# Kernel tuning notes

Hardware: AMD Instinct MI355X
Metric: run time of the kernel (lower is better)

## Reference

```python
import jax, jax.numpy as jnp
import numpy as np

B, N0, D0, N1, D1 = 128, 64, 32, 64, 32
K = 65  # depthwise conv kernel size
SCALE = 5.0
FOCUS = 3.0
EPS_Z = float(jnp.finfo(jnp.float32).eps)


def setup_inputs() -> dict:
    key = jax.random.key(0)
    k1, k2, k3, kw, kc, kb = jax.random.split(key, 6)
    x1 = jax.random.normal(k1, (B, N0, D0), dtype=jnp.float32)
    x2 = jax.random.normal(k2, (B, N0, D0), dtype=jnp.float32)
    x3 = jax.random.normal(k3, (B, N0, D0), dtype=jnp.float32)
    # kaiming_normal_ on W [N1, N0, D0, D1]: fan_in = N0*D0*D1 per torch default on 4D
    fan_in = N0 * D0 * D1
    W = jax.random.normal(kw, (N1, N0, D0, D1), dtype=jnp.float32) * np.sqrt(2.0 / fan_in)
    # Conv1d(N1*D1, N1*D1, K, groups=N1): weight [out_ch, in_ch/groups, K]
    cin_g = D1
    bound = 1.0 / np.sqrt(cin_g * K)
    conv_w = jax.random.uniform(kc, (N1 * D1, cin_g, K), dtype=jnp.float32, minval=-bound, maxval=bound)
    conv_b = jax.random.uniform(kb, (N1 * D1,), dtype=jnp.float32, minval=-bound, maxval=bound)
    return {"x1": x1, "x2": x2, "x3": x3, "W": W, "conv_w": conv_w, "conv_b": conv_b}


def _transform(x, W):
    # x: [B, N0, D0], W: [N1, N0, D0, D1] -> u: [B, N1*D1, N0]
    u = jnp.einsum('bji,kjiz->bkjz', x, W)        # [B, N1, N0, D1]
    u = jnp.transpose(u, (0, 1, 3, 2))             # [B, N1, D1, N0]
    return u.reshape(u.shape[0], N1 * D1, N0)


def _focus(u):
    # ReLU kernel + focusing-factor renormalization along last dim
    u = jax.nn.relu(u) + 1e-6
    u = u / SCALE
    n = jnp.linalg.norm(u, axis=-1, keepdims=True)
    up = u ** FOCUS
    return up / jnp.linalg.norm(up, axis=-1, keepdims=True) * n


def _squash(x, eps=1e-20):
    norm = jnp.linalg.norm(x, axis=-1, keepdims=True)
    coef = 1.0 - 1.0 / (jnp.exp(norm) + eps)
    return coef * (x / (norm + eps))


def reference(x1, x2, x3, W, conv_w, conv_b):
    u1 = _focus(_transform(x1, W))  # [B, N1*D1, N0]
    u2 = _focus(_transform(x2, W))
    u3 = _focus(_transform(x3, W))
    z = 1.0 / (jnp.einsum('bic,bc->bi', u1, u1.sum(axis=1)) + EPS_Z)  # [B, N1*D1]
    kv = jnp.einsum('bjc,bjd->bcd', u2, u3)                           # [B, N0, N0]
    x = jnp.einsum('bic,bcd,bi->bid', u1, kv, z)                      # [B, N1*D1, N0]
    # grouped (depthwise-per-capsule) conv1d, 'same' padding
    y = jax.lax.conv_general_dilated(
        x, conv_w, window_strides=(1,), padding=[(K // 2, K // 2)],
        dimension_numbers=('NCH', 'OIH', 'NCH'), feature_group_count=N1)
    y = y + conv_b[None, :, None]
    out = (x + y).sum(axis=-1).reshape(-1, N1, D1)  # [B, N1, D1]
    return _squash(out)
```

## Files before the change

### kernel.cpp

```cpp
#include <hip/hip_runtime.h>
#include <cstddef>

#define NB 128
#define NT 64
#define ND 32
#define NG 64
#define NC 2048
#define KW 65
#define EPSZ 1.1920928955078125e-07f

#define OFF_URAW 0ull
#define SZ_URAW  (3ull * NB * NT * NC)
#define OFF_F    (OFF_URAW + SZ_URAW)
#define SZ_F     (3ull * NB * NC)
#define OFF_S1   (OFF_F + SZ_F)
#define SZ_S1    ((unsigned long long)NB * NT)
#define OFF_KV   (OFF_S1 + SZ_S1)
#define SZ_KV    ((unsigned long long)NB * NT * NT)

__device__ __forceinline__ float foc(float v, float fv) {
  float u = (fmaxf(v, 0.f) + 1e-6f) * 0.2f;
  return u * u * u * fv;
}

__global__ __launch_bounds__(256) void k_transform(
    const float* __restrict__ x1, const float* __restrict__ x2,
    const float* __restrict__ x3, const float* __restrict__ W,
    float* __restrict__ uraw) {
  int bid = blockIdx.x;
  int j   = bid & 63;
  int nt  = (bid >> 6) & 15;
  int inp = bid >> 10;
  const float* x = (inp == 0) ? x1 : ((inp == 1) ? x2 : x3);
  float* uout = uraw + (size_t)inp * ((size_t)NB * NT * NC);

  __shared__ float as[32][132];
  __shared__ float bs[32][132];
  int tid = threadIdx.x;

  {
    int b = tid >> 1, h = tid & 1;
    const float* xp = x + ((size_t)b * NT + j) * ND + h * 16;
#pragma unroll
    for (int q = 0; q < 4; ++q) {
      float4 v = *reinterpret_cast<const float4*>(xp + q * 4);
      int i0 = h * 16 + q * 4;
      as[i0 + 0][b] = v.x; as[i0 + 1][b] = v.y;
      as[i0 + 2][b] = v.z; as[i0 + 3][b] = v.w;
    }
  }
  {
    int kk = tid >> 6, u = tid & 63;
    int i = u >> 1, h = u & 1;
    const float* wp = W + (((size_t)(nt * 4 + kk) * NT + j) * ND + i) * ND + h * 16;
#pragma unroll
    for (int q = 0; q < 4; ++q) {
      float4 v = *reinterpret_cast<const float4*>(wp + q * 4);
      int c0 = kk * 32 + h * 16 + q * 4;
      bs[i][c0 + 0] = v.x; bs[i][c0 + 1] = v.y;
      bs[i][c0 + 2] = v.z; bs[i][c0 + 3] = v.w;
    }
  }
  __syncthreads();

  int tm = tid & 15, tn = tid >> 4;
  int m0 = tm * 8, n0 = tn * 8;
  float acc[8][8];
#pragma unroll
  for (int a = 0; a < 8; ++a)
#pragma unroll
    for (int c = 0; c < 8; ++c) acc[a][c] = 0.f;

#pragma unroll 4
  for (int kk = 0; kk < 32; ++kk) {
    float4 a0 = *reinterpret_cast<const float4*>(&as[kk][m0]);
    float4 a1 = *reinterpret_cast<const float4*>(&as[kk][m0 + 4]);
    float4 b0 = *reinterpret_cast<const float4*>(&bs[kk][n0]);
    float4 b1 = *reinterpret_cast<const float4*>(&bs[kk][n0 + 4]);
    float av[8] = {a0.x, a0.y, a0.z, a0.w, a1.x, a1.y, a1.z, a1.w};
    float bv[8] = {b0.x, b0.y, b0.z, b0.w, b1.x, b1.y, b1.z, b1.w};
#pragma unroll
    for (int mi = 0; mi < 8; ++mi)
#pragma unroll
      for (int ni = 0; ni < 8; ++ni)
        acc[mi][ni] = fmaf(av[mi], bv[ni], acc[mi][ni]);
  }

#pragma unroll
  for (int mi = 0; mi < 8; ++mi) {
    float* cp = uout + ((size_t)(m0 + mi) * NT + j) * NC + nt * 128 + n0;
    float4 v0 = {acc[mi][0], acc[mi][1], acc[mi][2], acc[mi][3]};
    float4 v1 = {acc[mi][4], acc[mi][5], acc[mi][6], acc[mi][7]};
    *reinterpret_cast<float4*>(cp)     = v0;
    *reinterpret_cast<float4*>(cp + 4) = v1;
  }
}

__global__ __launch_bounds__(256) void k_factors(
    const float* __restrict__ uraw, float* __restrict__ f,
    float* __restrict__ s1) {
  int bid = blockIdx.x;
  int q = bid & 3, b = bid >> 2;
  const float* u = uraw + (size_t)b * ((size_t)NT * NC);
  int tid = threadIdx.x;
  int ch = q * 512 + tid * 2;

  float s2a = 0.f, s6a = 0.f, s2b = 0.f, s6b = 0.f;
  for (int t = 0; t < NT; ++t) {
    float2 v = *reinterpret_cast<const float2*>(u + (size_t)t * NC + ch);
    float ua = (fmaxf(v.x, 0.f) + 1e-6f) * 0.2f;
    float p2a = ua * ua, p3a = p2a * ua;
    s2a += p2a; s6a += p3a * p3a;
    float ub = (fmaxf(v.y, 0.f) + 1e-6f) * 0.2f;
    float p2b = ub * ub, p3b = p2b * ub;
    s2b += p2b; s6b += p3b * p3b;
  }
  float fa = sqrtf(s2a) / sqrtf(s6a);
  float fb = sqrtf(s2b) / sqrtf(s6b);
  float2 fv = {fa, fb};
  *reinterpret_cast<float2*>(f + (size_t)b * NC + ch) = fv;

  __shared__ float part[NT][4];
  int wid = tid >> 6, lane = tid & 63;
  for (int t = 0; t < NT; ++t) {
    float2 v = *reinterpret_cast<const float2*>(u + (size_t)t * NC + ch);
    float ua = (fmaxf(v.x, 0.f) + 1e-6f) * 0.2f;
    float ub = (fmaxf(v.y, 0.f) + 1e-6f) * 0.2f;
    float val = ua * ua * ua * fa + ub * ub * ub * fb;
#pragma unroll
    for (int m = 32; m >= 1; m >>= 1) val += __shfl_xor(val, m, 64);
    if (lane == 0) part[t][wid] = val;
  }
  __syncthreads();
  if (tid < NT)
    atomicAdd(&s1[b * NT + tid],
              part[tid][0] + part[tid][1] + part[tid][2] + part[tid][3]);
}

__global__ void k_zero(float* __restrict__ p, int n) {
  int i = blockIdx.x * blockDim.x + threadIdx.x;
  int stride = gridDim.x * blockDim.x;
  for (; i < n; i += stride) p[i] = 0.f;
}

__global__ __launch_bounds__(256) void k_kv(
    const float* __restrict__ uraw, float* __restrict__ kv) {
  int b = blockIdx.x >> 3, ks = blockIdx.x & 7;
  int tid = threadIdx.x;
  int wv = tid >> 6, lane = tid & 63;
  const float* u2 = uraw + ((size_t)NB + b) * ((size_t)NT * NC);
  const float* u3 = uraw + (2ull * NB + b) * ((size_t)NT * NC);

  __shared__ float L[2][64][32];
  __shared__ float fL[2][32];

  int q4 = tid & 7, tr = tid >> 3;
  int colf = tid >> 1, hf = tid & 1;
  int opf = colf >> 5, chf = colf & 31, c4f = chf >> 2, clf = chf & 3;
  int qr = wv >> 1, qc = wv & 1;
  int tm = lane >> 3, tn = lane & 7;

  float acc[4][4];
#pragma unroll
  for (int i = 0; i < 4; ++i)
#pragma unroll
    for (int j = 0; j < 4; ++j) acc[i][j] = 0.f;

  for (int chunk = 0; chunk < 8; ++chunk) {
    int ch0 = ks * 256 + chunk * 32;
    __syncthreads();
#pragma unroll
    for (int it = 0; it < 2; ++it) {
      int t = it * 32 + tr;
      int q4s = q4 ^ (t & 7) ^ (t >> 3);
      float4 v2 = *reinterpret_cast<const float4*>(u2 + (size_t)t * NC + ch0 + q4 * 4);
      float4 v3 = *reinterpret_cast<const float4*>(u3 + (size_t)t * NC + ch0 + q4 * 4);
      *reinterpret_cast<float4*>(&L[0][t][q4s * 4]) = v2;
      *reinterpret_cast<float4*>(&L[1][t][q4s * 4]) = v3;
    }
    __syncthreads();
    {
      float s2 = 0.f, s6 = 0.f;
#pragma unroll
      for (int k = 0; k < 32; ++k) {
        int t = hf * 32 + k;
        float v = L[opf][t][((c4f ^ (t & 7) ^ (t >> 3)) << 2) + clf];
        float uu = (fmaxf(v, 0.f) + 1e-6f) * 0.2f;
        float p2 = uu * uu; s2 += p2;
        float p3 = p2 * uu; s6 += p3 * p3;
      }
      s2 += __shfl_xor(s2, 1, 64);
      s6 += __shfl_xor(s6, 1, 64);
      if (hf == 0) fL[opf][chf] = sqrtf(s2) / sqrtf(s6);
    }
    __syncthreads();
    {
      float4 f2q = *reinterpret_cast<const float4*>(&fL[0][q4 * 4]);
      float4 f3q = *reinterpret_cast<const float4*>(&fL[1][q4 * 4]);
#pragma unroll
      for (int it = 0; it < 2; ++it) {
        int t = it * 32 + tr;
        int q4s = q4 ^ (t & 7) ^ (t >> 3);
        float* p2p = &L[0][t][q4s * 4];
        float* p3p = &L[1][t][q4s * 4];
        float4 v2 = *reinterpret_cast<const float4*>(p2p);
        float4 v3 = *reinterpret_cast<const float4*>(p3p);
        float4 w2 = {foc(v2.x, f2q.x), foc(v2.y, f2q.y), foc(v2.z, f2q.z), foc(v2.w, f2q.w)};
        float4 w3 = {foc(v3.x, f3q.x), foc(v3.y, f3q.y), foc(v3.z, f3q.z), foc(v3.w, f3q.w)};
        *reinterpret_cast<float4*>(p2p) = w2;
        *reinterpret_cast<float4*>(p3p) = w3;
      }
    }
    __syncthreads();
#pragma unroll
    for (int kp = 0; kp < 16; ++kp) {
      int qk = kp >> 1, h2 = (kp & 1) * 2;
      float2 af[4], bf[4];
#pragma unroll
      for (int i = 0; i < 4; ++i) {
        int t1 = qr * 32 + tm * 4 + i;
        af[i] = *reinterpret_cast<const float2*>(
            &L[0][t1][((qk ^ (t1 & 7) ^ (t1 >> 3)) << 2) + h2]);
      }
#pragma unroll
      for (int j = 0; j < 4; ++j) {
        int t2 = qc * 32 + tn * 4 + j;
        bf[j] = *reinterpret_cast<const float2*>(
            &L[1][t2][((qk ^ (t2 & 7) ^ (t2 >> 3)) << 2) + h2]);
      }
#pragma unroll
      for (int i = 0; i < 4; ++i)
#pragma unroll
        for (int j = 0; j < 4; ++j)
          acc[i][j] = fmaf(af[i].y, bf[j].y, fmaf(af[i].x, bf[j].x, acc[i][j]));
    }
  }

  float* kvp = kv + (size_t)b * (NT * NT);
#pragma unroll
  for (int i = 0; i < 4; ++i)
#pragma unroll
    for (int j = 0; j < 4; ++j)
      atomicAdd(&kvp[(qr * 32 + tm * 4 + i) * 64 + qc * 32 + tn * 4 + j],
                acc[i][j]);
}

__global__ __launch_bounds__(64) void k_cwt(
    const float* __restrict__ cw, float* __restrict__ cwt) {
  int o = blockIdx.x;
  int tid = threadIdx.x;
  __shared__ float row[32 * KW];
  for (int i = tid; i < 32 * KW; i += 64) row[i] = cw[(size_t)o * (32 * KW) + i];
  __syncthreads();
  int jj = tid, j = jj + 1;
  for (int ci = 0; ci < 32; ++ci) {
    float v = 0.f;
    if (j <= 32) v -= row[ci * KW + j + 32];
    if (j >= 32 && j <= 63) v += row[ci * KW + j - 32];
    if (j == 64) {
      float s = 0.f;
      for (int k = 32; k <= 64; ++k) s += row[ci * KW + k];
      v += s;
    }
    cwt[(size_t)o * 2048 + ci * 64 + jj] = v;
  }
}

__global__ __launch_bounds__(256) void k_pre(
    const float* __restrict__ uraw, const float* __restrict__ f,
    const float* __restrict__ kvg, const float* __restrict__ s1g,
    float* __restrict__ pre) {
  int b = blockIdx.x >> 3, q = blockIdx.x & 7;
  int chbase = q * 256;
  const float* u1 = uraw + (size_t)b * ((size_t)NT * NC);
  const float* f1 = f + (size_t)b * NC;
  int tid = threadIdx.x;

  __shared__ float kvpreL[64][68];
  __shared__ float s1L[64];
  __shared__ float utL[64][132];

#pragma unroll
  for (int qq = 0; qq < 16; ++qq) {
    int i = tid + qq * 256;
    kvpreL[i >> 6][i & 63] = kvg[(size_t)b * (NT * NT) + i];
  }
  if (tid < 64) s1L[tid] = s1g[b * NT + tid];
  __syncthreads();
  if (tid < 64) {
    float run = 0.f;
    for (int t2 = 0; t2 < 64; ++t2) {
      run += kvpreL[tid][t2];
      kvpreL[tid][t2] = run;
    }
  }

  int cg = tid >> 3, tg = tid & 7;
  for (int tile = 0; tile < 2; ++tile) {
    int ch0 = chbase + tile * 128;
    __syncthreads();
    {
      int t = tid >> 2, c4 = tid & 3;
      const float* up = u1 + (size_t)t * NC + ch0 + c4 * 32;
      const float* fp = f1 + ch0 + c4 * 32;
#pragma unroll
      for (int qq = 0; qq < 8; ++qq) {
        float4 v  = *reinterpret_cast<const float4*>(up + qq * 4);
        float4 fv = *reinterpret_cast<const float4*>(fp + qq * 4);
        float vv[4] = {v.x, v.y, v.z, v.w};
        float ff[4] = {fv.x, fv.y, fv.z, fv.w};
#pragma unroll
        for (int r = 0; r < 4; ++r) {
          float uu = (fmaxf(vv[r], 0.f) + 1e-6f) * 0.2f;
          utL[t][c4 * 33 + qq * 4 + r] = uu * uu * uu * ff[r];
        }
      }
    }
    __syncthreads();

    int cl = cg * 4;
    int sk = (cl >> 5) * 33 + (cl & 31);
    float acc[4][8];
#pragma unroll
    for (int r = 0; r < 4; ++r)
#pragma unroll
      for (int c = 0; c < 8; ++c) acc[r][c] = 0.f;
    float accz[4] = {0.f, 0.f, 0.f, 0.f};

#pragma unroll 4
    for (int t1 = 0; t1 < 64; ++t1) {
      float4 a = *reinterpret_cast<const float4*>(&utL[t1][sk]);
      float s = s1L[t1];
      float4 k0 = *reinterpret_cast<const float4*>(&kvpreL[t1][tg * 8]);
      float4 k1 = *reinterpret_cast<const float4*>(&kvpreL[t1][tg * 8 + 4]);
      float aa[4] = {a.x, a.y, a.z, a.w};
      float kk[8] = {k0.x, k0.y, k0.z, k0.w, k1.x, k1.y, k1.z, k1.w};
#pragma unroll
      for (int r = 0; r < 4; ++r) {
        accz[r] = fmaf(aa[r], s, accz[r]);
#pragma unroll
        for (int c = 0; c < 8; ++c)
          acc[r][c] = fmaf(aa[r], kk[c], acc[r][c]);
      }
    }
#pragma unroll
    for (int r = 0; r < 4; ++r) {
      float z = 1.f / (accz[r] + EPSZ);
      float* pp = pre + ((size_t)b * NC + ch0 + cl + r) * 64 + tg * 8;
      float4 o0 = {acc[r][0] * z, acc[r][1] * z, acc[r][2] * z, acc[r][3] * z};
      float4 o1 = {acc[r][4] * z, acc[r][5] * z, acc[r][6] * z, acc[r][7] * z};
      *reinterpret_cast<float4*>(pp)     = o0;
      *reinterpret_cast<float4*>(pp + 4) = o1;
    }
  }
}

__global__ __launch_bounds__(256) void k_gemm(
    const float* __restrict__ pre, const float* __restrict__ cwt,
    const float* __restrict__ cb, float* __restrict__ out) {
  int g = blockIdx.x >> 2, bq = blockIdx.x & 3;
  int b0 = bq * 32;
  int tid = threadIdx.x;
  int oh = tid & 15, bh = tid >> 4;

  __shared__ float preL[32][68];
  __shared__ float cwtL[32][68];

  float a00 = 0.f, a01 = 0.f, a10 = 0.f, a11 = 0.f;
  float xs00 = 0.f, xs01 = 0.f, xs10 = 0.f, xs11 = 0.f;

  for (int kc = 0; kc < 32; ++kc) {
    __syncthreads();
    {
      int r8 = tid >> 3, s8 = tid & 7;
      const float* ps = pre + ((size_t)(b0 + r8) * NC + g * 32) * 64 + kc * 64 + s8 * 8;
      float4 p0 = *reinterpret_cast<const float4*>(ps);
      float4 p1 = *reinterpret_cast<const float4*>(ps + 4);
      *reinterpret_cast<float4*>(&preL[r8][s8 * 8])     = p0;
      *reinterpret_cast<float4*>(&preL[r8][s8 * 8 + 4]) = p1;
      const float* cs = cwt + (size_t)(g * 32 + r8) * 2048 + kc * 64 + s8 * 8;
      float4 c0 = *reinterpret_cast<const float4*>(cs);
      float4 c1 = *reinterpret_cast<const float4*>(cs + 4);
      *reinterpret_cast<float4*>(&cwtL[r8][s8 * 8])     = c0;
      *reinterpret_cast<float4*>(&cwtL[r8][s8 * 8 + 4]) = c1;
    }
    __syncthreads();

    if (kc == oh)      { xs00 = preL[bh][63]; xs10 = preL[bh + 16][63]; }
    if (kc == oh + 16) { xs01 = preL[bh][63]; xs11 = preL[bh + 16][63]; }

#pragma unroll
    for (int kk = 0; kk < 64; kk += 4) {
      float4 p0 = *reinterpret_cast<const float4*>(&preL[bh][kk]);
      float4 p1 = *reinterpret_cast<const float4*>(&preL[bh + 16][kk]);
      float4 c0 = *reinterpret_cast<const float4*>(&cwtL[oh][kk]);
      float4 c1 = *reinterpret_cast<const float4*>(&cwtL[oh + 16][kk]);
      a00 = fmaf(p0.x, c0.x, a00); a00 = fmaf(p0.y, c0.y, a00);
      a00 = fmaf(p0.z, c0.z, a00); a00 = fmaf(p0.w, c0.w, a00);
      a01 = fmaf(p0.x, c1.x, a01); a01 = fmaf(p0.y, c1.y, a01);
      a01 = fmaf(p0.z, c1.z, a01); a01 = fmaf(p0.w, c1.w, a01);
      a10 = fmaf(p1.x, c0.x, a10); a10 = fmaf(p1.y, c0.y, a10);
      a10 = fmaf(p1.z, c0.z, a10); a10 = fmaf(p1.w, c0.w, a10);
      a11 = fmaf(p1.x, c1.x, a11); a11 = fmaf(p1.y, c1.y, a11);
      a11 = fmaf(p1.z, c1.z, a11); a11 = fmaf(p1.w, c1.w, a11);
    }
  }

  float cb0 = cb[g * 32 + oh], cb1 = cb[g * 32 + oh + 16];
  float v00 = a00 + xs00 + 64.f * cb0;
  float v01 = a01 + xs01 + 64.f * cb1;
  float v10 = a10 + xs10 + 64.f * cb0;
  float v11 = a11 + xs11 + 64.f * cb1;

  float sqA = v00 * v00 + v01 * v01;
  float sqB = v10 * v10 + v11 * v11;
#pragma unroll
  for (int m = 8; m >= 1; m >>= 1) {
    sqA += __shfl_xor(sqA, m, 16);
    sqB += __shfl_xor(sqB, m, 16);
  }
  float nA = sqrtf(sqA), nB = sqrtf(sqB);
  float cA = 1.f - 1.f / (expf(nA) + 1e-20f);
  float cB = 1.f - 1.f / (expf(nB) + 1e-20f);
  float iA = cA / (nA + 1e-20f), iB = cB / (nB + 1e-20f);

  size_t baseA = ((size_t)(b0 + bh) * NG + g) * ND;
  size_t baseB = ((size_t)(b0 + bh + 16) * NG + g) * ND;
  out[baseA + oh]      = v00 * iA;
  out[baseA + oh + 16] = v01 * iA;
  out[baseB + oh]      = v10 * iB;
  out[baseB + oh + 16] = v11 * iB;
}

extern "C" void kernel_launch(void* const* d_in, const int* in_sizes, int n_in,
                              void* d_out, int out_size, void* d_ws, size_t ws_size,
                              hipStream_t stream) {
  const float* x1 = (const float*)d_in[0];
  const float* x2 = (const float*)d_in[1];
  const float* x3 = (const float*)d_in[2];
  const float* W  = (const float*)d_in[3];
  const float* cw = (const float*)d_in[4];
  const float* cb = (const float*)d_in[5];
  float* out = (float*)d_out;

  float* ws   = (float*)d_ws;
  float* uraw = ws + OFF_URAW;
  float* f    = ws + OFF_F;
  float* s1   = ws + OFF_S1;
  float* kv   = ws + OFF_KV;
  float* pre  = uraw + (size_t)NB * NT * NC;
  float* cwt  = uraw + 2ull * NB * NT * NC;

  k_transform<<<3072, 256, 0, stream>>>(x1, x2, x3, W, uraw);
  k_zero<<<256, 256, 0, stream>>>(s1, (int)(SZ_S1 + SZ_KV));
  k_factors<<<512, 256, 0, stream>>>(uraw, f, s1);
  k_kv<<<1024, 256, 0, stream>>>(uraw, kv);
  k_cwt<<<2048, 64, 0, stream>>>(cw, cwt);
  k_pre<<<1024, 256, 0, stream>>>(uraw, f, kv, s1, pre);
  k_gemm<<<256, 256, 0, stream>>>(pre, cwt, cb, out);
}
```

Before: 412.0 us.

## Store transformed activations as fp16 and restructure the kv factor computation

The large intermediate u tensor, the per-input transform output for all three inputs, is now written as packed half2 values instead of fp32. Every consumer (factors, kv, pre) converts back to float on load, which halves the global write and read traffic on the dominant buffer. The kv kernel also drops the XOR-swizzled shared layout for a padded one, and computes the focus normalisation factors with a 16-lane shuffle reduction over four channels per thread. The workspace is re-laid-out so that cwt and the other small buffers sit after the smaller half-precision buffer. The cost is fp16 rounding of pre-activation values before the cubic focus step, which adds numerical error.

Result: faster. 365.3 us (-11.3%).

```diff
diff --git a/kernel.cpp b/kernel.cpp
--- a/kernel.cpp
+++ b/kernel.cpp
@@ -1,4 +1,5 @@
 #include <hip/hip_runtime.h>
+#include <hip/hip_fp16.h>
 #include <cstddef>
 
 #define NB 128
@@ -9,14 +10,9 @@
 #define KW 65
 #define EPSZ 1.1920928955078125e-07f
 
-#define OFF_URAW 0ull
-#define SZ_URAW  (3ull * NB * NT * NC)
-#define OFF_F    (OFF_URAW + SZ_URAW)
-#define SZ_F     (3ull * NB * NC)
-#define OFF_S1   (OFF_F + SZ_F)
-#define SZ_S1    ((unsigned long long)NB * NT)
-#define OFF_KV   (OFF_S1 + SZ_S1)
-#define SZ_KV    ((unsigned long long)NB * NT * NT)
+#define URAW_HALVES   (3ull * NB * NT * NC)
+#define URAW_FLOATS   (URAW_HALVES / 2)
+#define PRE_OFF       ((size_t)NB * NT * NC / 2)
 
 __device__ __forceinline__ float foc(float v, float fv) {
   float u = (fmaxf(v, 0.f) + 1e-6f) * 0.2f;
@@ -26,13 +22,13 @@
 __global__ __launch_bounds__(256) void k_transform(
     const float* __restrict__ x1, const float* __restrict__ x2,
     const float* __restrict__ x3, const float* __restrict__ W,
-    float* __restrict__ uraw) {
+    __half* __restrict__ uraw) {
   int bid = blockIdx.x;
   int j   = bid & 63;
   int nt  = (bid >> 6) & 15;
   int inp = bid >> 10;
   const float* x = (inp == 0) ? x1 : ((inp == 1) ? x2 : x3);
-  float* uout = uraw + (size_t)inp * ((size_t)NB * NT * NC);
+  __half* uout = uraw + (size_t)inp * ((size_t)NB * NT * NC);
 
   __shared__ float as[32][132];
   __shared__ float bs[32][132];
@@ -88,26 +84,28 @@
 
 #pragma unroll
   for (int mi = 0; mi < 8; ++mi) {
-    float* cp = uout + ((size_t)(m0 + mi) * NT + j) * NC + nt * 128 + n0;
-    float4 v0 = {acc[mi][0], acc[mi][1], acc[mi][2], acc[mi][3]};
-    float4 v1 = {acc[mi][4], acc[mi][5], acc[mi][6], acc[mi][7]};
-    *reinterpret_cast<float4*>(cp)     = v0;
-    *reinterpret_cast<float4*>(cp + 4) = v1;
+    __half* cp = uout + ((size_t)(m0 + mi) * NT + j) * NC + nt * 128 + n0;
+    __half2 hh[4];
+    hh[0] = __floats2half2_rn(acc[mi][0], acc[mi][1]);
+    hh[1] = __floats2half2_rn(acc[mi][2], acc[mi][3]);
+    hh[2] = __floats2half2_rn(acc[mi][4], acc[mi][5]);
+    hh[3] = __floats2half2_rn(acc[mi][6], acc[mi][7]);
+    *reinterpret_cast<float4*>(cp) = *reinterpret_cast<const float4*>(hh);
   }
 }
 
 __global__ __launch_bounds__(256) void k_factors(
-    const float* __restrict__ uraw, float* __restrict__ f,
+    const __half* __restrict__ uraw, float* __restrict__ f,
     float* __restrict__ s1) {
   int bid = blockIdx.x;
   int q = bid & 3, b = bid >> 2;
-  const float* u = uraw + (size_t)b * ((size_t)NT * NC);
+  const __half* u = uraw + (size_t)b * ((size_t)NT * NC);
   int tid = threadIdx.x;
   int ch = q * 512 + tid * 2;
 
   float s2a = 0.f, s6a = 0.f, s2b = 0.f, s6b = 0.f;
   for (int t = 0; t < NT; ++t) {
-    float2 v = *reinterpret_cast<const float2*>(u + (size_t)t * NC + ch);
+    float2 v = __half22float2(*reinterpret_cast<const __half2*>(u + (size_t)t * NC + ch));
     float ua = (fmaxf(v.x, 0.f) + 1e-6f) * 0.2f;
     float p2a = ua * ua, p3a = p2a * ua;
     s2a += p2a; s6a += p3a * p3a;
@@ -123,7 +121,7 @@
   __shared__ float part[NT][4];
   int wid = tid >> 6, lane = tid & 63;
   for (int t = 0; t < NT; ++t) {
-    float2 v = *reinterpret_cast<const float2*>(u + (size_t)t * NC + ch);
+    float2 v = __half22float2(*reinterpret_cast<const __half2*>(u + (size_t)t * NC + ch));
     float ua = (fmaxf(v.x, 0.f) + 1e-6f) * 0.2f;
     float ub = (fmaxf(v.y, 0.f) + 1e-6f) * 0.2f;
     float val = ua * ua * ua * fa + ub * ub * ub * fb;
@@ -144,20 +142,21 @@
 }
 
 __global__ __launch_bounds__(256) void k_kv(
-    const float* __restrict__ uraw, float* __restrict__ kv) {
+    const __half* __restrict__ uraw, float* __restrict__ kv) {
   int b = blockIdx.x >> 3, ks = blockIdx.x & 7;
   int tid = threadIdx.x;
   int wv = tid >> 6, lane = tid & 63;
-  const float* u2 = uraw + ((size_t)NB + b) * ((size_t)NT * NC);
-  const float* u3 = uraw + (2ull * NB + b) * ((size_t)NT * NC);
-
-  __shared__ float L[2][64][32];
+  const __half* u2 = uraw + ((size_t)NB + b) * ((size_t)NT * NC);
+  const __half* u3 = uraw + (2ull * NB + b) * ((size_t)NT * NC);
+
+  __shared__ float L[2][64][34];
   __shared__ float fL[2][32];
 
-  int q4 = tid & 7, tr = tid >> 3;
-  int colf = tid >> 1, hf = tid & 1;
-  int opf = colf >> 5, chf = colf & 31, c4f = chf >> 2, clf = chf & 3;
-  int qr = wv >> 1, qc = wv & 1;
+  int oc = tid & 3, ts = tid >> 2;
+  int qcf = lane >> 4, tseg = lane & 15;
+  int qqf = wv * 4 + qcf;
+  int opf = qqf >> 3, c4f = qqf & 7;
+  int qr = wv >> 1, qcw = wv & 1;
   int tm = lane >> 3, tn = lane & 7;
 
   float acc[4][4];
@@ -169,65 +168,76 @@
   for (int chunk = 0; chunk < 8; ++chunk) {
     int ch0 = ks * 256 + chunk * 32;
     __syncthreads();
-#pragma unroll
-    for (int it = 0; it < 2; ++it) {
-      int t = it * 32 + tr;
-      int q4s = q4 ^ (t & 7) ^ (t >> 3);
-      float4 v2 = *reinterpret_cast<const float4*>(u2 + (size_t)t * NC + ch0 + q4 * 4);
-      float4 v3 = *reinterpret_cast<const float4*>(u3 + (size_t)t * NC + ch0 + q4 * 4);
-      *reinterpret_cast<float4*>(&L[0][t][q4s * 4]) = v2;
-      *reinterpret_cast<float4*>(&L[1][t][q4s * 4]) = v3;
-    }
-    __syncthreads();
     {
-      float s2 = 0.f, s6 = 0.f;
-#pragma unroll
-      for (int k = 0; k < 32; ++k) {
-        int t = hf * 32 + k;
-        float v = L[opf][t][((c4f ^ (t & 7) ^ (t >> 3)) << 2) + clf];
-        float uu = (fmaxf(v, 0.f) + 1e-6f) * 0.2f;
-        float p2 = uu * uu; s2 += p2;
-        float p3 = p2 * uu; s6 += p3 * p3;
+      float4 r2 = *reinterpret_cast<const float4*>(u2 + (size_t)ts * NC + ch0 + oc * 8);
+      float4 r3 = *reinterpret_cast<const float4*>(u3 + (size_t)ts * NC + ch0 + oc * 8);
+      const __half2* h2p = reinterpret_cast<const __half2*>(&r2);
+      const __half2* h3p = reinterpret_cast<const __half2*>(&r3);
+      float* d2 = &L[0][ts][oc * 8];
+      float* d3 = &L[1][ts][oc * 8];
+#pragma unroll
+      for (int k = 0; k < 4; ++k) {
+        float2 a = __half22float2(h2p[k]);
+        float2 c = __half22float2(h3p[k]);
+        *reinterpret_cast<float2*>(d2 + 2 * k) = a;
+        *reinterpret_cast<float2*>(d3 + 2 * k) = c;
       }
-      s2 += __shfl_xor(s2, 1, 64);
-      s6 += __shfl_xor(s6, 1, 64);
-      if (hf == 0) fL[opf][chf] = sqrtf(s2) / sqrtf(s6);
     }
     __syncthreads();
     {
-      float4 f2q = *reinterpret_cast<const float4*>(&fL[0][q4 * 4]);
-      float4 f3q = *reinterpret_cast<const float4*>(&fL[1][q4 * 4]);
-#pragma unroll
-      for (int it = 0; it < 2; ++it) {
-        int t = it * 32 + tr;
-        int q4s = q4 ^ (t & 7) ^ (t >> 3);
-        float* p2p = &L[0][t][q4s * 4];
-        float* p3p = &L[1][t][q4s * 4];
-        float4 v2 = *reinterpret_cast<const float4*>(p2p);
-        float4 v3 = *reinterpret_cast<const float4*>(p3p);
-        float4 w2 = {foc(v2.x, f2q.x), foc(v2.y, f2q.y), foc(v2.z, f2q.z), foc(v2.w, f2q.w)};
-        float4 w3 = {foc(v3.x, f3q.x), foc(v3.y, f3q.y), foc(v3.z, f3q.z), foc(v3.w, f3q.w)};
-        *reinterpret_cast<float4*>(p2p) = w2;
-        *reinterpret_cast<float4*>(p3p) = w3;
+      float s2[4] = {0.f, 0.f, 0.f, 0.f}, s6[4] = {0.f, 0.f, 0.f, 0.f};
+#pragma unroll
+      for (int r = 0; r < 4; ++r) {
+        int t = tseg + 16 * r;
+        float2 p0 = *reinterpret_cast<const float2*>(&L[opf][t][c4f * 4]);
+        float2 p1 = *reinterpret_cast<const float2*>(&L[opf][t][c4f * 4 + 2]);
+        float vv[4] = {p0.x, p0.y, p1.x, p1.y};
+#pragma unroll
+        for (int c = 0; c < 4; ++c) {
+          float uu = (fmaxf(vv[c], 0.f) + 1e-6f) * 0.2f;
+          float p2 = uu * uu; s2[c] += p2;
+          float p3 = p2 * uu; s6[c] += p3 * p3;
+        }
       }
+#pragma unroll
+      for (int m = 8; m >= 1; m >>= 1)
+#pragma unroll
+        for (int c = 0; c < 4; ++c) {
+          s2[c] += __shfl_xor(s2[c], m, 16);
+          s6[c] += __shfl_xor(s6[c], m, 16);
+        }
+      if (tseg == 0)
+#pragma unroll
+        for (int c = 0; c < 4; ++c)
+          fL[opf][c4f * 4 + c] = sqrtf(s2[c]) / sqrtf(s6[c]);
+    }
+    __syncthreads();
+    {
+      float fa[8], fb[8];
+#pragma unroll
+      for (int k = 0; k < 8; ++k) { fa[k] = fL[0][oc * 8 + k]; fb[k] = fL[1][oc * 8 + k]; }
+      float* d2 = &L[0][ts][oc * 8];
+      float* d3 = &L[1][ts][oc * 8];
+#pragma unroll
+      for (int k = 0; k < 4; ++k) {
+        float2 a = *reinterpret_cast<const float2*>(d2 + 2 * k);
+        float2 c = *reinterpret_cast<const float2*>(d3 + 2 * k);
+        a.x = foc(a.x, fa[2 * k]); a.y = foc(a.y, fa[2 * k + 1]);
+        c.x = foc(c.x, fb[2 * k]); c.y = foc(c.y, fb[2 * k + 1]);
+        *reinterpret_cast<float2*>(d2 + 2 * k) = a;
+        *reinterpret_cast<float2*>(d3 + 2 * k) = c;
+      }
     }
     __syncthreads();
 #pragma unroll
     for (int kp = 0; kp < 16; ++kp) {
-      int qk = kp >> 1, h2 = (kp & 1) * 2;
       float2 af[4], bf[4];
 #pragma unroll
-      for (int i = 0; i < 4; ++i) {
-        int t1 = qr * 32 + tm * 4 + i;
-        af[i] = *reinterpret_cast<const float2*>(
-            &L[0][t1][((qk ^ (t1 & 7) ^ (t1 >> 3)) << 2) + h2]);
-      }
-#pragma unroll
-      for (int j = 0; j < 4; ++j) {
-        int t2 = qc * 32 + tn * 4 + j;
-        bf[j] = *reinterpret_cast<const float2*>(
-            &L[1][t2][((qk ^ (t2 & 7) ^ (t2 >> 3)) << 2) + h2]);
-      }
+      for (int i = 0; i < 4; ++i)
+        af[i] = *reinterpret_cast<const float2*>(&L[0][qr * 32 + tm * 4 + i][kp * 2]);
+#pragma unroll
+      for (int j = 0; j < 4; ++j)
+        bf[j] = *reinterpret_cast<const float2*>(&L[1][qcw * 32 + tn * 4 + j][kp * 2]);
 #pragma unroll
       for (int i = 0; i < 4; ++i)
 #pragma unroll
@@ -241,7 +251,7 @@
   for (int i = 0; i < 4; ++i)
 #pragma unroll
     for (int j = 0; j < 4; ++j)
-      atomicAdd(&kvp[(qr * 32 + tm * 4 + i) * 64 + qc * 32 + tn * 4 + j],
+      atomicAdd(&kvp[(qr * 32 + tm * 4 + i) * 64 + qcw * 32 + tn * 4 + j],
                 acc[i][j]);
 }
 
@@ -267,12 +277,12 @@
 }
 
 __global__ __launch_bounds__(256) void k_pre(
-    const float* __restrict__ uraw, const float* __restrict__ f,
+    const __half* __restrict__ uraw, const float* __restrict__ f,
     const float* __restrict__ kvg, const float* __restrict__ s1g,
     float* __restrict__ pre) {
   int b = blockIdx.x >> 3, q = blockIdx.x & 7;
   int chbase = q * 256;
-  const float* u1 = uraw + (size_t)b * ((size_t)NT * NC);
+  const __half* u1 = uraw + (size_t)b * ((size_t)NT * NC);
   const float* f1 = f + (size_t)b * NC;
   int tid = threadIdx.x;
 
@@ -301,18 +311,22 @@
     __syncthreads();
     {
       int t = tid >> 2, c4 = tid & 3;
-      const float* up = u1 + (size_t)t * NC + ch0 + c4 * 32;
+      const __half* up = u1 + (size_t)t * NC + ch0 + c4 * 32;
       const float* fp = f1 + ch0 + c4 * 32;
 #pragma unroll
-      for (int qq = 0; qq < 8; ++qq) {
-        float4 v  = *reinterpret_cast<const float4*>(up + qq * 4);
-        float4 fv = *reinterpret_cast<const float4*>(fp + qq * 4);
-        float vv[4] = {v.x, v.y, v.z, v.w};
-        float ff[4] = {fv.x, fv.y, fv.z, fv.w};
+      for (int qq = 0; qq < 4; ++qq) {
+        float4 raw = *reinterpret_cast<const float4*>(up + qq * 8);
+        const __half2* hp = reinterpret_cast<const __half2*>(&raw);
+        float4 fv0 = *reinterpret_cast<const float4*>(fp + qq * 8);
+        float4 fv1 = *reinterpret_cast<const float4*>(fp + qq * 8 + 4);
+        float ff[8] = {fv0.x, fv0.y, fv0.z, fv0.w, fv1.x, fv1.y, fv1.z, fv1.w};
 #pragma unroll
         for (int r = 0; r < 4; ++r) {
-          float uu = (fmaxf(vv[r], 0.f) + 1e-6f) * 0.2f;
-          utL[t][c4 * 33 + qq * 4 + r] = uu * uu * uu * ff[r];
+          float2 uv = __half22float2(hp[r]);
+          float ua = (fmaxf(uv.x, 0.f) + 1e-6f) * 0.2f;
+          float ub = (fmaxf(uv.y, 0.f) + 1e-6f) * 0.2f;
+          utL[t][c4 * 33 + qq * 8 + r * 2]     = ua * ua * ua * ff[r * 2];
+          utL[t][c4 * 33 + qq * 8 + r * 2 + 1] = ub * ub * ub * ff[r * 2 + 1];
         }
       }
     }
@@ -444,15 +458,15 @@
   float* out = (float*)d_out;
 
   float* ws   = (float*)d_ws;
-  float* uraw = ws + OFF_URAW;
-  float* f    = ws + OFF_F;
-  float* s1   = ws + OFF_S1;
-  float* kv   = ws + OFF_KV;
-  float* pre  = uraw + (size_t)NB * NT * NC;
-  float* cwt  = uraw + 2ull * NB * NT * NC;
+  __half* uraw = (__half*)d_ws;
+  float* pre  = ws + PRE_OFF;
+  float* f    = ws + URAW_FLOATS;
+  float* s1   = f + (size_t)NB * NC;
+  float* kv   = s1 + (size_t)NB * NT;
+  float* cwt  = kv + (size_t)NB * NT * NT;
 
   k_transform<<<3072, 256, 0, stream>>>(x1, x2, x3, W, uraw);
-  k_zero<<<256, 256, 0, stream>>>(s1, (int)(SZ_S1 + SZ_KV));
+  k_zero<<<256, 256, 0, stream>>>(s1, (int)(NB * NT + NB * NT * NT));
   k_factors<<<512, 256, 0, stream>>>(uraw, f, s1);
   k_kv<<<1024, 256, 0, stream>>>(uraw, kv);
   k_cwt<<<2048, 64, 0, stream>>>(cw, cwt);
```
